# Kernel tuning notes

Hardware: AMD Instinct MI355X
Metric: run time of the kernel (lower is better)

## Reference

```python
import jax, jax.numpy as jnp
import numpy as np

# Scalar quantization params (QLinear __init__ args)
FEATURE_BITWIDTH = 8
WEIGHT_BITWIDTH = 8
INPUT_ZERO_POINT = -3
OUTPUT_ZERO_POINT = -5
INPUT_SCALE = 0.05
OUTPUT_SCALE = 0.1
QMIN = -(1 << (FEATURE_BITWIDTH - 1))   # -128
QMAX = (1 << (FEATURE_BITWIDTH - 1)) - 1  # 127

M, K, N = 8192, 4096, 4096


def float_to_fixed_point(x, bitwidth):
    """Represent x (0 < x < 1) as int_scale * 2^-frac_bits with int_scale
    in [2^(bitwidth-2), 2^(bitwidth-1)) (mantissa fits in signed `bitwidth` bits)."""
    frac_bits = (bitwidth - 1 - jnp.ceil(jnp.log2(x))).astype(jnp.int32)
    int_scale = jnp.round(x * jnp.exp2(frac_bits.astype(jnp.float32))).astype(jnp.int32)
    return int_scale, frac_bits


def setup_inputs() -> dict:
    key = jax.random.key(0)
    k1, k2, k3, k4 = jax.random.split(key, 4)
    qinput = jax.random.randint(k1, (M, K), -128, 128, dtype=jnp.int8)
    qweight = jax.random.randint(k2, (N, K), -128, 128, dtype=jnp.int8)
    qbias = jax.random.randint(k3, (N,), -(1 << 16), 1 << 16, dtype=jnp.int32)
    # per-output-channel weight scale; keeps folded scale in (0, 1)
    weight_scale = jax.random.uniform(k4, (N,), jnp.float32, 0.002, 0.02)
    return {"qinput": qinput, "qweight": qweight, "qbias": qbias,
            "weight_scale": weight_scale}


def reference(qinput, qweight, qbias, weight_scale):
    w32 = qweight.astype(jnp.int32)                      # [N, K]
    # Qbias' = qbias - sum_k(qweight) * Zin  (bias shift folding input zero point)
    shifted_qbias = qbias - w32.sum(axis=1) * INPUT_ZERO_POINT  # [N]
    # int32 GEMM: [M, K] @ [K, N] + bias
    acc = qinput.astype(jnp.int32) @ w32.T + shifted_qbias[None, :]  # [M, N]
    # fixed-point requantization: (acc * int_scale) >> frac_bits + Zout
    folded_scale = INPUT_SCALE * weight_scale / OUTPUT_SCALE         # [N], in (0,1)
    int_scale, frac_bits = float_to_fixed_point(folded_scale, FEATURE_BITWIDTH)
    # widen to int64 for the multiply so the (acc * int_scale) product cannot wrap
    prod = acc.astype(jnp.int64) * int_scale.astype(jnp.int64)[None, :]
    scaled = jnp.right_shift(prod, frac_bits.astype(jnp.int64)[None, :])  # arithmetic >>
    out = scaled + OUTPUT_ZERO_POINT
    return jnp.clip(out, QMIN, QMAX).astype(jnp.int8)
```

## Files before the change

### kernel.cpp

```cpp
#include <hip/hip_runtime.h>
#include <cstdint>
#include <cstddef>

#define M_DIM 8192
#define N_DIM 4096
#define K_DIM 4096

#define BM 128
#define BN 128
#define BK 128

#define BM2 256
#define BN2 256
#define BK2 128
#define NKT (K_DIM / BK2)

typedef int int32x4  __attribute__((ext_vector_type(4)));
typedef int int32x16 __attribute__((ext_vector_type(16)));


typedef __attribute__((address_space(1))) const void* gas_cptr;
typedef __attribute__((address_space(3))) void* las_ptr;

__device__ __forceinline__ void async_copy16(const void* g, void* l) {
    __builtin_amdgcn_global_load_lds((gas_cptr)g, (las_ptr)l, 16, 0, 0);
}

__device__ __forceinline__ int32x4 pack16(const int* p) {
    const int32x4* v = (const int32x4*)p;
    int32x4 w0 = v[0], w1 = v[1], w2 = v[2], w3 = v[3];
    int32x4 r;
    r.x = (w0.x & 0xFF) | ((w0.y & 0xFF) << 8) | ((w0.z & 0xFF) << 16) | (w0.w << 24);
    r.y = (w1.x & 0xFF) | ((w1.y & 0xFF) << 8) | ((w1.z & 0xFF) << 16) | (w1.w << 24);
    r.z = (w2.x & 0xFF) | ((w2.y & 0xFF) << 8) | ((w2.z & 0xFF) << 16) | (w2.w << 24);
    r.w = (w3.x & 0xFF) | ((w3.y & 0xFF) << 8) | ((w3.z & 0xFF) << 16) | (w3.w << 24);
    return r;
}

__global__ void ql_detect_kernel(const int* a, const int* b, int* ws) {
    int t = threadIdx.x;
    int fa = 0, fb = 0;
    for (int i = t; i < 4096; i += 64) {
        int va = a[i]; if (va > 127 || va < -128) fa = 1;
        int vb = b[i]; if (vb > 127 || vb < -128) fb = 1;
    }
    unsigned long long ba = __ballot(fa);
    unsigned long long bb = __ballot(fb);
    if (t == 0) { ws[0] = ba ? 1 : 0; ws[1] = bb ? 1 : 0; }
}

#define PACK_WBLK 4096
#define PACK_ABLK 8192
__global__ __launch_bounds__(256)
void ql_pack2_kernel(const void* wsrc, int* wdst, const void* asrc, int* adst,
                     const int* qbias, const float* wscale, int* ws) {
    __shared__ int red[4];
    const int fA = __builtin_amdgcn_readfirstlane(ws[0]);
    const int fW = __builtin_amdgcn_readfirstlane(ws[1]);
    const int bid = blockIdx.x;
    const int tid = threadIdx.x;
    if (bid < PACK_WBLK) {
        if (fW) return;
        const int n = bid;
        const int32x4* src = (const int32x4*)wsrc + (size_t)n * 1024;
        int* dst = wdst + (size_t)n * 1024;
        int s = 0;
#pragma unroll
        for (int k = 0; k < 4; ++k) {
            const int i = k * 256 + tid;
            int32x4 v = src[i];
            s += v.x + v.y + v.z + v.w;
            dst[i] = (v.x & 0xFF) | ((v.y & 0xFF) << 8) | ((v.z & 0xFF) << 16) | (v.w << 24);
        }
#pragma unroll
        for (int off = 32; off > 0; off >>= 1) s += __shfl_down(s, off, 64);
        if ((tid & 63) == 0) red[tid >> 6] = s;
        __syncthreads();
        if (tid == 0) {
            const int st = red[0] + red[1] + red[2] + red[3];
            ws[16 + n] = qbias[n] + 3 * st;
            float folded = (0.05f * wscale[n]) / 0.1f;
            int fbits = (int)(7.0f - ceilf(log2f(folded)));
            int isc = (int)rintf(folded * exp2f((float)fbits));
            ws[16 + N_DIM + n] = isc;
            ws[16 + 2 * N_DIM + n] = fbits;
        }
    } else {
        if (fA) return;
        const long base = (long)(bid - PACK_WBLK) * 1024;
        const int32x4* src = (const int32x4*)asrc + base;
        int* dst = adst + base;
#pragma unroll
        for (int k = 0; k < 4; ++k) {
            const int i = k * 256 + tid;
            int32x4 v = src[i];
            dst[i] = (v.x & 0xFF) | ((v.y & 0xFF) << 8) | ((v.z & 0xFF) << 16) | (v.w << 24);
        }
    }
}

__global__ void ql_prep8_kernel(const void* worig, const int* qbias,
                                const float* wscale, int* ws) {
    const int fb = __builtin_amdgcn_readfirstlane(ws[1]);
    if (!fb) return;

    const int lane = threadIdx.x & 63;
    const int wid  = threadIdx.x >> 6;
    const int n = blockIdx.x * 4 + wid;

    const int32x4* row = (const int32x4*)((const int8_t*)worig + (size_t)n * K_DIM);
    int s = 0;
    for (int c = lane; c < K_DIM / 16; c += 64) {
        int32x4 v = row[c];
#pragma unroll
        for (int j = 0; j < 4; ++j) {
            int w = (j == 0) ? v.x : (j == 1) ? v.y : (j == 2) ? v.z : v.w;
            s += (int)(int8_t)(w) + (int)(int8_t)(w >> 8)
               + (int)(int8_t)(w >> 16) + (w >> 24);
        }
    }
#pragma unroll
    for (int off = 32; off > 0; off >>= 1) s += __shfl_down(s, off, 64);

    if (lane == 0) {
        ws[16 + n] = qbias[n] + 3 * s;
        float folded = (0.05f * wscale[n]) / 0.1f;
        int fbits = (int)(7.0f - ceilf(log2f(folded)));
        int isc = (int)rintf(folded * exp2f((float)fbits));
        ws[16 + N_DIM + n] = isc;
        ws[16 + 2 * N_DIM + n] = fbits;
    }
}

__global__ void ql_prep_kernel(const void* wptr, const int* qbias,
                               const float* wscale, int* ws) {
    const int lane = threadIdx.x & 63;
    const int wid  = threadIdx.x >> 6;
    const int n = blockIdx.x * 4 + wid;
    const int b8 = __builtin_amdgcn_readfirstlane(ws[1]);

    int s = 0;
    if (b8) {
        const int32x4* row = (const int32x4*)((const int8_t*)wptr + (size_t)n * K_DIM);
        for (int c = lane; c < K_DIM / 16; c += 64) {
            int32x4 v = row[c];
#pragma unroll
            for (int j = 0; j < 4; ++j) {
                int w = (j == 0) ? v.x : (j == 1) ? v.y : (j == 2) ? v.z : v.w;
                s += (int)(int8_t)(w) + (int)(int8_t)(w >> 8)
                   + (int)(int8_t)(w >> 16) + (w >> 24);
            }
        }
    } else {
        const int32x4* row = (const int32x4*)((const int*)wptr + (size_t)n * K_DIM);
        for (int c = lane; c < K_DIM / 4; c += 64) {
            int32x4 v = row[c];
            s += v.x + v.y + v.z + v.w;
        }
    }
#pragma unroll
    for (int off = 32; off > 0; off >>= 1) s += __shfl_down(s, off, 64);

    if (lane == 0) {
        ws[16 + n] = qbias[n] + 3 * s;
        float folded = (0.05f * wscale[n]) / 0.1f;
        int fbits = (int)(7.0f - ceilf(log2f(folded)));
        int isc = (int)rintf(folded * exp2f((float)fbits));
        ws[16 + N_DIM + n] = isc;
        ws[16 + 2 * N_DIM + n] = fbits;
    }
}

__device__ __forceinline__ void ql_epilogue(int32x4 acc[4][4], const int* ws,
                                            int* out, int bm, int bn,
                                            int wm, int wn, int qm, int qh) {
    const int* qb  = ws + 16;
    const int* isc = ws + 16 + N_DIM;
    const int* fbt = ws + 16 + 2 * N_DIM;
#pragma unroll
    for (int j = 0; j < 4; ++j) {
        const int n_g = bn * BN + wn + j * 16 + qm;
        const int b0 = qb[n_g];
        const int s0 = isc[n_g];
        const int f0 = fbt[n_g];
#pragma unroll
        for (int i = 0; i < 4; ++i) {
            const int m_base = bm * BM + wm + i * 16 + qh * 4;
#pragma unroll
            for (int r = 0; r < 4; ++r) {
                int v = ((r == 0) ? acc[i][j].x : (r == 1) ? acc[i][j].y
                        : (r == 2) ? acc[i][j].z : acc[i][j].w) + b0;
                long long p = (long long)v * (long long)s0;
                int o = (int)(p >> f0) - 5;
                o = o < -128 ? -128 : (o > 127 ? 127 : o);
                out[(size_t)(m_base + r) * N_DIM + n_g] = o;
            }
        }
    }
}


#define TILE4(BUF, TT, DOST) do { \
    _Pragma("unroll") for (int i = 0; i < 4; ++i) af[0][i] = LA[BUF][baseAe[0] + i * 256]; \
    _Pragma("unroll") for (int j = 0; j < 4; ++j) bf[0][j] = LB[BUF][baseBe[0] + j * 256]; \
    if (DOST) { \
        _Pragma("unroll") for (int h = 0; h < 8; ++h) { \
            async_copy16(gA + (size_t)((TT) + 1) * 128 + (size_t)h * 131072, \
                         &LA[(BUF) ^ 1][h * 256 + t]); \
            async_copy16(gB + (size_t)((TT) + 1) * 128 + (size_t)h * 131072, \
                         &LB[(BUF) ^ 1][h * 256 + t]); \
        } \
    } \
    _Pragma("unroll") for (int kc = 0; kc < 4; ++kc) { \
        if (kc < 3) { \
            _Pragma("unroll") for (int i = 0; i < 4; ++i) \
                af[kc + 1][i] = LA[BUF][baseAe[kc + 1] + i * 256]; \
            _Pragma("unroll") for (int j = 0; j < 4; ++j) \
                bf[kc + 1][j] = LB[BUF][baseBe[kc + 1] + j * 256]; \
        } \
        __builtin_amdgcn_s_setprio(1); \
        _Pragma("unroll") for (int i = 0; i < 4; ++i) \
        _Pragma("unroll") for (int j = 0; j < 4; ++j) \
            acc[i][j] = __builtin_amdgcn_mfma_i32_32x32x32_i8( \
                af[kc][i], bf[kc][j], acc[i][j], 0, 0, 0); \
        __builtin_amdgcn_s_setprio(0); \
    } \
    __syncthreads(); \
} while (0)

__global__ __launch_bounds__(256, 1)
void ql_gemm8_kernel(const void* a0, const int8_t* a8,
                     const void* b0, const int8_t* w8,
                     const int* ws, int* out) {
    __shared__ int32x4 LA[2][2048];
    __shared__ int32x4 LB[2][2048];

    const int fa = __builtin_amdgcn_readfirstlane(ws[0]);
    const int fb = __builtin_amdgcn_readfirstlane(ws[1]);
    const int8_t* aptr = fa ? (const int8_t*)a0 : a8;
    const int8_t* bptr = fb ? (const int8_t*)b0 : w8;

    const int t    = threadIdx.x;
    const int lane = t & 63;
    const int wid  = t >> 6;
    const int wr   = wid >> 1;
    const int wc   = wid & 1;
    const int l31  = lane & 31;
    const int hi   = lane >> 5;

    const int flat = blockIdx.y * gridDim.x + blockIdx.x;
    const int xcd  = flat & 7;
    const int lid  = flat >> 3;
    const int g    = lid >> 5;
    const int r    = lid & 31;
    const int bm   = xcd * 4 + g * 2 + (r & 1);
    const int bn   = r >> 1;

    const int arow0 = bm * BM2;
    const int brow0 = bn * BN2;

    const int fr = (lane & 7) ^ ((l31 >> 3) & 3);
    int baseAe[4], baseBe[4];
#pragma unroll
    for (int kc = 0; kc < 4; ++kc) {
        const int phys = (kc * 2 + hi) ^ fr;
        baseAe[kc] = (wr * 128 + l31) * 8 + phys;
        baseBe[kc] = (wc * 128 + l31) * 8 + phys;
    }

    const int colg = (t & 7) ^ ((t >> 3) & 7) ^ ((t >> 6) & 3);
    const int8_t* gA = aptr + (size_t)(arow0 + (t >> 3)) * K_DIM + colg * 16;
    const int8_t* gB = bptr + (size_t)(brow0 + (t >> 3)) * K_DIM + colg * 16;

    int32x16 acc[4][4] = {};
    int32x4 af[4][4], bf[4][4];

#pragma unroll
    for (int h = 0; h < 8; ++h) {
        async_copy16(gA + (size_t)h * 131072, &LA[0][h * 256 + t]);
        async_copy16(gB + (size_t)h * 131072, &LB[0][h * 256 + t]);
    }
    __syncthreads();

#pragma unroll 1
    for (int T = 0; T < NKT - 2; T += 2) {
        TILE4(0, T, true);
        TILE4(1, T + 1, true);
    }
    TILE4(0, NKT - 2, true);
    TILE4(1, NKT - 1, false);

    const int* qb  = ws + 16;
    const int* isc = ws + 16 + N_DIM;
    const int* fbt = ws + 16 + 2 * N_DIM;
#pragma unroll
    for (int j = 0; j < 4; ++j) {
        const int n_g = bn * BN2 + wc * 128 + j * 32 + l31;
        const int b0r = qb[n_g];
        const int s0r = isc[n_g];
        const int f0r = fbt[n_g];
#pragma unroll
        for (int i = 0; i < 4; ++i) {
            const int m0 = bm * BM2 + wr * 128 + i * 32 + hi * 4;
#pragma unroll
            for (int reg = 0; reg < 16; ++reg) {
                const int row = (reg & 3) + 8 * (reg >> 2);
                int v = acc[i][j][reg] + b0r;
                long long p = (long long)v * (long long)s0r;
                int o = (int)(p >> f0r) - 5;
                o = o < -128 ? -128 : (o > 127 ? 127 : o);
                __builtin_nontemporal_store(o, &out[(size_t)(m0 + row) * N_DIM + n_g]);
            }
        }
    }
}

__global__ __launch_bounds__(256)
void ql_gemm_fb_kernel(const void* aptr, const void* bptr, const int* ws, int* out) {
    __shared__ int32x4 Als[BM * BK / 16];
    __shared__ int32x4 Bls[BN * BK / 16];

    const int a8 = __builtin_amdgcn_readfirstlane(ws[0]);
    const int b8 = __builtin_amdgcn_readfirstlane(ws[1]);

    const int t    = threadIdx.x;
    const int lane = t & 63;
    const int wid  = t >> 6;
    const int bn = blockIdx.x;
    const int bm = blockIdx.y;

    const int wm = (wid >> 1) * 64;
    const int wn = (wid & 1) * 64;
    const int qm = lane & 15;
    const int qh = lane >> 4;

    int32x4 acc[4][4] = {};

    for (int kt = 0; kt < K_DIM / BK; ++kt) {
        __syncthreads();
        const int k0 = kt * BK;
#pragma unroll
        for (int r = 0; r < 4; ++r) {
            const int c    = r * 256 + t;
            const int row  = c >> 3;
            const int colg = (c & 7) ^ (row & 7);
            const size_t offA = (size_t)(bm * BM + row) * K_DIM + k0 + colg * 16;
            const size_t offB = (size_t)(bn * BN + row) * K_DIM + k0 + colg * 16;
            if (a8) async_copy16((const int8_t*)aptr + offA, &Als[c]);
            else    Als[c] = pack16((const int*)aptr + offA);
            if (b8) async_copy16((const int8_t*)bptr + offB, &Bls[c]);
            else    Bls[c] = pack16((const int*)bptr + offB);
        }
        __syncthreads();

#pragma unroll
        for (int s = 0; s < 2; ++s) {
            const int colk = s * 4 + qh;
            int32x4 af[4], bf[4];
#pragma unroll
            for (int i = 0; i < 4; ++i) {
                const int ra = wm + i * 16 + qm;
                const int rb = wn + i * 16 + qm;
                af[i] = Als[ra * 8 + (colk ^ (ra & 7))];
                bf[i] = Bls[rb * 8 + (colk ^ (rb & 7))];
            }
#pragma unroll
            for (int i = 0; i < 4; ++i)
#pragma unroll
                for (int j = 0; j < 4; ++j)
                    acc[i][j] = __builtin_amdgcn_mfma_i32_16x16x64_i8(
                        af[i], bf[j], acc[i][j], 0, 0, 0);
        }
    }
    ql_epilogue(acc, ws, out, bm, bn, wm, wn, qm, qh);
}

extern "C" void kernel_launch(void* const* d_in, const int* in_sizes, int n_in,
                              void* d_out, int out_size, void* d_ws, size_t ws_size,
                              hipStream_t stream) {
    const void* qin    = d_in[0];
    const void* qwt    = d_in[1];
    const int* qbias   = (const int*)d_in[2];
    const float* wscal = (const float*)d_in[3];
    int* ws  = (int*)d_ws;
    int* out = (int*)d_out;

    hipLaunchKernelGGL(ql_detect_kernel, dim3(1), dim3(64), 0, stream,
                       (const int*)qin, (const int*)qwt, ws);

    const size_t need = 65536 + (size_t)M_DIM * K_DIM + (size_t)N_DIM * K_DIM;
    if (ws_size >= need) {
        int8_t* a8 = (int8_t*)d_ws + 65536;
        int8_t* w8 = a8 + (size_t)M_DIM * K_DIM;
        hipLaunchKernelGGL(ql_pack2_kernel, dim3(PACK_WBLK + PACK_ABLK), dim3(256),
                           0, stream, qwt, (int*)w8, qin, (int*)a8, qbias, wscal, ws);
        hipLaunchKernelGGL(ql_prep8_kernel, dim3(N_DIM / 4), dim3(256), 0, stream,
                           qwt, qbias, wscal, ws);
        hipLaunchKernelGGL(ql_gemm8_kernel, dim3(N_DIM / BN2, M_DIM / BM2), dim3(256),
                           0, stream, qin, a8, qwt, w8, ws, out);
    } else {
        hipLaunchKernelGGL(ql_prep_kernel, dim3(N_DIM / 4), dim3(256), 0, stream,
                           qwt, qbias, wscal, ws);
        hipLaunchKernelGGL(ql_gemm_fb_kernel, dim3(N_DIM / BN, M_DIM / BM), dim3(256), 0, stream,
                           qin, qwt, ws, out);
    }
}
```

Before: 425.0 us.

## Shrink GEMM tile to 128x128 with two blocks per CU and simpler k-loop

Reduces the int8 MFMA GEMM block tile from 256x256 to 128x128, halving LDS buffers and accumulators so two blocks can be resident per CU. The software-pipelined register prefetch across k-chunks is replaced by loading all fragments up front and then issuing MFMAs. The XCD-aware block remapping is adjusted for the larger grid. This trades per-block data reuse (more global/LDS traffic per FLOP) for occupancy and latency hiding.

```diff
diff --git a/kernel.cpp b/kernel.cpp
--- a/kernel.cpp
+++ b/kernel.cpp
@@ -10,10 +10,10 @@
 #define BN 128
 #define BK 128
 
-#define BM2 256
-#define BN2 256
-#define BK2 128
-#define NKT (K_DIM / BK2)
+#define BM3 128
+#define BN3 128
+#define BK3 128
+#define NKT (K_DIM / BK3)
 
 typedef int int32x4  __attribute__((ext_vector_type(4)));
 typedef int int32x16 __attribute__((ext_vector_type(16)));
@@ -200,40 +200,39 @@
 }
 
 
-#define TILE4(BUF, TT, DOST) do { \
-    _Pragma("unroll") for (int i = 0; i < 4; ++i) af[0][i] = LA[BUF][baseAe[0] + i * 256]; \
-    _Pragma("unroll") for (int j = 0; j < 4; ++j) bf[0][j] = LB[BUF][baseBe[0] + j * 256]; \
-    if (DOST) { \
-        _Pragma("unroll") for (int h = 0; h < 8; ++h) { \
-            async_copy16(gA + (size_t)((TT) + 1) * 128 + (size_t)h * 131072, \
-                         &LA[(BUF) ^ 1][h * 256 + t]); \
-            async_copy16(gB + (size_t)((TT) + 1) * 128 + (size_t)h * 131072, \
-                         &LB[(BUF) ^ 1][h * 256 + t]); \
-        } \
+#define STAGE3(BUF, TT) do { \
+    _Pragma("unroll") for (int r3 = 0; r3 < 4; ++r3) { \
+        async_copy16(gA + (size_t)(TT) * 128 + (size_t)r3 * 131072, \
+                     &LA[BUF][r3 * 256 + t]); \
+        async_copy16(gB + (size_t)(TT) * 128 + (size_t)r3 * 131072, \
+                     &LB[BUF][r3 * 256 + t]); \
     } \
+} while (0)
+
+#define TILE3(BUF, TT) do { \
+    if ((TT) + 1 < NKT) { STAGE3((BUF) ^ 1, (TT) + 1); } \
     _Pragma("unroll") for (int kc = 0; kc < 4; ++kc) { \
-        if (kc < 3) { \
-            _Pragma("unroll") for (int i = 0; i < 4; ++i) \
-                af[kc + 1][i] = LA[BUF][baseAe[kc + 1] + i * 256]; \
-            _Pragma("unroll") for (int j = 0; j < 4; ++j) \
-                bf[kc + 1][j] = LB[BUF][baseBe[kc + 1] + j * 256]; \
-        } \
-        __builtin_amdgcn_s_setprio(1); \
-        _Pragma("unroll") for (int i = 0; i < 4; ++i) \
-        _Pragma("unroll") for (int j = 0; j < 4; ++j) \
-            acc[i][j] = __builtin_amdgcn_mfma_i32_32x32x32_i8( \
-                af[kc][i], bf[kc][j], acc[i][j], 0, 0, 0); \
-        __builtin_amdgcn_s_setprio(0); \
+        _Pragma("unroll") for (int i = 0; i < 2; ++i) \
+            af[i][kc] = LA[BUF][baseAe[kc] + i * 256]; \
+        _Pragma("unroll") for (int j = 0; j < 2; ++j) \
+            bf[j][kc] = LB[BUF][baseBe[kc] + j * 256]; \
     } \
+    __builtin_amdgcn_s_setprio(1); \
+    _Pragma("unroll") for (int j = 0; j < 2; ++j) \
+    _Pragma("unroll") for (int kc = 0; kc < 4; ++kc) \
+    _Pragma("unroll") for (int i = 0; i < 2; ++i) \
+        acc[i][j] = __builtin_amdgcn_mfma_i32_32x32x32_i8( \
+            af[i][kc], bf[j][kc], acc[i][j], 0, 0, 0); \
+    __builtin_amdgcn_s_setprio(0); \
     __syncthreads(); \
 } while (0)
 
-__global__ __launch_bounds__(256, 1)
+__global__ __launch_bounds__(256, 2)
 void ql_gemm8_kernel(const void* a0, const int8_t* a8,
                      const void* b0, const int8_t* w8,
                      const int* ws, int* out) {
-    __shared__ int32x4 LA[2][2048];
-    __shared__ int32x4 LB[2][2048];
+    __shared__ int32x4 LA[2][1024];
+    __shared__ int32x4 LB[2][1024];
 
     const int fa = __builtin_amdgcn_readfirstlane(ws[0]);
     const int fb = __builtin_amdgcn_readfirstlane(ws[1]);
@@ -251,57 +250,51 @@
     const int flat = blockIdx.y * gridDim.x + blockIdx.x;
     const int xcd  = flat & 7;
     const int lid  = flat >> 3;
-    const int g    = lid >> 5;
-    const int r    = lid & 31;
-    const int bm   = xcd * 4 + g * 2 + (r & 1);
+    const int g    = lid >> 6;
+    const int r    = lid & 63;
+    const int bm   = xcd * 8 + g * 2 + (r & 1);
     const int bn   = r >> 1;
 
-    const int arow0 = bm * BM2;
-    const int brow0 = bn * BN2;
+    const int arow0 = bm * BM3;
+    const int brow0 = bn * BN3;
 
     const int fr = (lane & 7) ^ ((l31 >> 3) & 3);
     int baseAe[4], baseBe[4];
 #pragma unroll
     for (int kc = 0; kc < 4; ++kc) {
         const int phys = (kc * 2 + hi) ^ fr;
-        baseAe[kc] = (wr * 128 + l31) * 8 + phys;
-        baseBe[kc] = (wc * 128 + l31) * 8 + phys;
+        baseAe[kc] = (wr * 64 + l31) * 8 + phys;
+        baseBe[kc] = (wc * 64 + l31) * 8 + phys;
     }
 
     const int colg = (t & 7) ^ ((t >> 3) & 7) ^ ((t >> 6) & 3);
     const int8_t* gA = aptr + (size_t)(arow0 + (t >> 3)) * K_DIM + colg * 16;
     const int8_t* gB = bptr + (size_t)(brow0 + (t >> 3)) * K_DIM + colg * 16;
 
-    int32x16 acc[4][4] = {};
-    int32x4 af[4][4], bf[4][4];
-
-#pragma unroll
-    for (int h = 0; h < 8; ++h) {
-        async_copy16(gA + (size_t)h * 131072, &LA[0][h * 256 + t]);
-        async_copy16(gB + (size_t)h * 131072, &LB[0][h * 256 + t]);
-    }
+    int32x16 acc[2][2] = {};
+    int32x4 af[2][4], bf[2][4];
+
+    STAGE3(0, 0);
     __syncthreads();
 
 #pragma unroll 1
-    for (int T = 0; T < NKT - 2; T += 2) {
-        TILE4(0, T, true);
-        TILE4(1, T + 1, true);
-    }
-    TILE4(0, NKT - 2, true);
-    TILE4(1, NKT - 1, false);
+    for (int T = 0; T < NKT; T += 2) {
+        TILE3(0, T);
+        TILE3(1, T + 1);
+    }
 
     const int* qb  = ws + 16;
     const int* isc = ws + 16 + N_DIM;
     const int* fbt = ws + 16 + 2 * N_DIM;
 #pragma unroll
-    for (int j = 0; j < 4; ++j) {
-        const int n_g = bn * BN2 + wc * 128 + j * 32 + l31;
+    for (int j = 0; j < 2; ++j) {
+        const int n_g = bn * BN3 + wc * 64 + j * 32 + l31;
         const int b0r = qb[n_g];
         const int s0r = isc[n_g];
         const int f0r = fbt[n_g];
 #pragma unroll
-        for (int i = 0; i < 4; ++i) {
-            const int m0 = bm * BM2 + wr * 128 + i * 32 + hi * 4;
+        for (int i = 0; i < 2; ++i) {
+            const int m0 = bm * BM3 + wr * 64 + i * 32 + hi * 4;
 #pragma unroll
             for (int reg = 0; reg < 16; ++reg) {
                 const int row = (reg & 3) + 8 * (reg >> 2);
@@ -396,7 +389,7 @@
                            0, stream, qwt, (int*)w8, qin, (int*)a8, qbias, wscal, ws);
         hipLaunchKernelGGL(ql_prep8_kernel, dim3(N_DIM / 4), dim3(256), 0, stream,
                            qwt, qbias, wscal, ws);
-        hipLaunchKernelGGL(ql_gemm8_kernel, dim3(N_DIM / BN2, M_DIM / BM2), dim3(256),
+        hipLaunchKernelGGL(ql_gemm8_kernel, dim3(N_DIM / BN3, M_DIM / BM3), dim3(256),
                            0, stream, qin, a8, qwt, w8, ws, out);
     } else {
         hipLaunchKernelGGL(ql_prep_kernel, dim3(N_DIM / 4), dim3(256), 0, stream,
```

Measured after the change: 451.4 us. 6.2% more time.
